# Optimization experiments

Measured on AMD Instinct MI355X. Metric: run time of the kernel, lower is better.

Reference implementation:

```python
import jax, jax.numpy as jnp
import numpy as np

B, N, T = 8, 8192, 2048
CW, DW = 1024, 256  # encoder_width (c_dim), decoder hidden_size
NBLK = 5
EPS = 1e-5


def setup_inputs() -> dict:
    key = jax.random.key(0)
    ks = jax.random.split(key, 32)
    pts = jax.random.normal(ks[0], (B, N, 3), dtype=jnp.float32) * 5.0
    drop = jax.random.bernoulli(ks[1], 0.3, (B, N))
    pts = pts.at[..., 0].set(jnp.where(drop, -100.0, pts[..., 0]))
    rgb = jax.random.uniform(ks[2], (B, N, 3), dtype=jnp.float32)
    query_coords = jax.random.normal(ks[3], (B, T, 3), dtype=jnp.float32) * 5.0
    s = lambda k, shp: jax.random.normal(k, shp, dtype=jnp.float32) * 0.02
    inp = {
        "pts": pts, "rgb": rgb, "query_coords": query_coords,
        # DumbPointnet: pointwise MLP (6->CW->CW) + max pool over points
        "enc_W1": s(ks[4], (6, CW)), "enc_b1": jnp.zeros((CW,), jnp.float32),
        "enc_W2": s(ks[5], (CW, CW)), "enc_b2": jnp.zeros((CW,), jnp.float32),
        # DecoderBatchNorm
        "fc_p_W": s(ks[6], (3, DW)), "fc_p_b": jnp.zeros((DW,), jnp.float32),
        "blk_Wg0": s(ks[7], (NBLK, CW, DW)), "blk_bg0": jnp.ones((NBLK, DW), jnp.float32),
        "blk_Wb0": s(ks[8], (NBLK, CW, DW)), "blk_bb0": jnp.zeros((NBLK, DW), jnp.float32),
        "blk_W0": s(ks[9], (NBLK, DW, DW)), "blk_b0": jnp.zeros((NBLK, DW), jnp.float32),
        "blk_Wg1": s(ks[10], (NBLK, CW, DW)), "blk_bg1": jnp.ones((NBLK, DW), jnp.float32),
        "blk_Wb1": s(ks[11], (NBLK, CW, DW)), "blk_bb1": jnp.zeros((NBLK, DW), jnp.float32),
        "blk_W1": s(ks[12], (NBLK, DW, DW)), "blk_b1": jnp.zeros((NBLK, DW), jnp.float32),
        "bn_Wg": s(ks[13], (CW, DW)), "bn_bg": jnp.ones((DW,), jnp.float32),
        "bn_Wb": s(ks[14], (CW, DW)), "bn_bb": jnp.zeros((DW,), jnp.float32),
        "fc_out_W": s(ks[15], (DW, 1)), "fc_out_b": jnp.zeros((1,), jnp.float32),
    }
    return inp


def _cbn(x, c, Wg, bg, Wb, bb):
    # Conditional BatchNorm1d (training-mode batch stats, affine=False core BN).
    # x: (B,T,F), c: (B,CW)
    mean = x.mean(axis=(0, 1))
    var = x.var(axis=(0, 1))
    xn = (x - mean) * jax.lax.rsqrt(var + EPS)
    gamma = c @ Wg + bg  # (B,F)
    beta = c @ Wb + bb
    return gamma[:, None, :] * xn + beta[:, None, :]


def _forward(pts, rgb, query_coords,
             enc_W1, enc_b1, enc_W2, enc_b2,
             fc_p_W, fc_p_b,
             blk_Wg0, blk_bg0, blk_Wb0, blk_bb0, blk_W0, blk_b0,
             blk_Wg1, blk_bg1, blk_Wb1, blk_bb1, blk_W1, blk_b1,
             bn_Wg, bn_bg, bn_Wb, bn_bb, fc_out_W, fc_out_b):
    mask = pts[..., 0] > -50.0  # (B,N) ragged validity mask
    # 99th-percentile of per-point norms over valid points (torch kthvalue semantics,
    # detached via .item() in the original -> stop_gradient).
    nrm = jnp.where(mask, jnp.linalg.norm(pts, axis=-1), jnp.inf)  # (B,N)
    nrm_sorted = jnp.sort(nrm, axis=-1)
    n_valid = mask.sum(axis=-1)  # (B,)
    k = 1 + jnp.round(0.99 * (n_valid - 1).astype(jnp.float32)).astype(jnp.int32)
    p99 = jnp.take_along_axis(nrm_sorted, (k - 1)[:, None], axis=-1)  # (B,1)
    p99 = jax.lax.stop_gradient(p99)
    pts_n = pts / p99[..., None]
    qc = query_coords / p99[..., None]
    # Encoder: pointwise MLP on [pts_n, rgb], masked max-pool over points
    x = jnp.concatenate([pts_n, rgb], axis=-1)  # (B,N,6)
    h = jax.nn.relu(x @ enc_W1 + enc_b1)
    h = jax.nn.relu(h @ enc_W2 + enc_b2)
    h = jnp.where(mask[..., None], h, -jnp.inf)
    c = h.max(axis=1)  # (B,CW)
    # Decoder: fc_p + 5 conditional-BN resnet blocks + final CBN head
    net = qc @ fc_p_W + fc_p_b  # (B,T,DW)
    for i in range(NBLK):
        dx = jax.nn.relu(_cbn(net, c, blk_Wg0[i], blk_bg0[i], blk_Wb0[i], blk_bb0[i])) @ blk_W0[i] + blk_b0[i]
        dx = jax.nn.relu(_cbn(dx, c, blk_Wg1[i], blk_bg1[i], blk_Wb1[i], blk_bb1[i])) @ blk_W1[i] + blk_b1[i]
        net = net + dx
    out = jax.nn.relu(_cbn(net, c, bn_Wg, bn_bg, bn_Wb, bn_bb)) @ fc_out_W + fc_out_b
    return out[..., 0]  # (B,T) logits


def reference(pts, rgb, query_coords,
              enc_W1, enc_b1, enc_W2, enc_b2,
              fc_p_W, fc_p_b,
              blk_Wg0, blk_bg0, blk_Wb0, blk_bb0, blk_W0, blk_b0,
              blk_Wg1, blk_bg1, blk_Wb1, blk_bb1, blk_W1, blk_b1,
              bn_Wg, bn_bg, bn_Wb, bn_bb, fc_out_W, fc_out_b):
    return _forward(pts, rgb, query_coords,
                    enc_W1, enc_b1, enc_W2, enc_b2,
                    fc_p_W, fc_p_b,
                    blk_Wg0, blk_bg0, blk_Wb0, blk_bb0, blk_W0, blk_b0,
                    blk_Wg1, blk_bg1, blk_Wb1, blk_bb1, blk_W1, blk_b1,
                    bn_Wg, bn_bg, bn_Wb, bn_bb, fc_out_W, fc_out_b)
```

## Files before the change

### kernel.cpp

```cpp
#include <hip/hip_runtime.h>
#include <hip/hip_bf16.h>

#define NB   8
#define NPTS 8192
#define NT   2048
#define CWID 1024
#define DWID 256
#define NPBLK 256

using f32x4  = __attribute__((ext_vector_type(4))) float;
using bf16x8 = __attribute__((ext_vector_type(8))) __bf16;
using bf16x4 = __attribute__((ext_vector_type(4))) __bf16;

#define OFF_INV    0u
#define OFF_C      66560u
#define OFF_GB     99328u
#define OFF_STATS  279552u
#define OFF_W2T    1048576u
#define OFF_WT     3145728u
#define OFF_GBP    4456448u
#define OFF_PART   7340032u
#define OFF_IDX    8388608u
#define OFF_NV     8650752u
#define OFF_NET    19922944u
#define OFF_DX     36700160u
#define OFF_H1     19922944u
#define OFF_H1F    67108864u
#define WS_NEEDED  53477376u
#define WS_BIG     201326592u

__device__ __forceinline__ void async_copy16(const void* g, void* l) {
  __builtin_amdgcn_global_load_lds(
      (const __attribute__((address_space(1))) unsigned int*)g,
      (__attribute__((address_space(3))) unsigned int*)l, 16, 0, 0);
}

__global__ __launch_bounds__(1024) void k_p99(
    const float* __restrict__ pts, float* __restrict__ inv_p99,
    int* __restrict__ idx, int* __restrict__ nv, float* __restrict__ c)
{
  const int b = blockIdx.x;
  const int t = threadIdx.x;
  __shared__ unsigned int keys[NPTS];
  __shared__ int whist[16][256];
  __shared__ int hist[256];
  __shared__ int s_cnt, s_kleft;
  __shared__ unsigned int s_prefix;

  c[b*CWID + t] = 0.f;
  if (t == 0) s_cnt = 0;
  __syncthreads();

  for (int n = t; n < NPTS; n += 1024) {
    const float x = pts[(b*NPTS + n)*3 + 0];
    const float y = pts[(b*NPTS + n)*3 + 1];
    const float z = pts[(b*NPTS + n)*3 + 2];
    const bool v = x > -50.f;
    unsigned int key = 0x7F800000u;
    if (v) {
      key = __float_as_uint(sqrtf(x*x + y*y + z*z));
      const int slot = atomicAdd(&s_cnt, 1);
      idx[b*NPTS + slot] = n;
    }
    keys[n] = key;
  }
  __syncthreads();
  if (t == 0) {
    nv[b] = s_cnt;
    s_kleft = 1 + (int)rintf(0.99f * (float)(s_cnt - 1));
    s_prefix = 0u;
  }
  __syncthreads();

  const int w = t >> 6;
  for (int pass = 0; pass < 4; ++pass) {
    const int shift = 24 - 8*pass;
    const unsigned int pref = s_prefix;
    for (int i = t; i < 16*256; i += 1024) ((int*)whist)[i] = 0;
    __syncthreads();
    for (int n = t; n < NPTS; n += 1024) {
      const unsigned int key = keys[n];
      const bool m = (pass == 0) || ((key >> (shift + 8)) == (pref >> (shift + 8)));
      if (m) atomicAdd(&whist[w][(key >> shift) & 255], 1);
    }
    __syncthreads();
    if (t < 256) { int h = 0; for (int ww = 0; ww < 16; ++ww) h += whist[ww][t]; hist[t] = h; }
    __syncthreads();
    if (t < 64) {
      const int kl = s_kleft;
      const int s0 = hist[t*4+0], s1 = hist[t*4+1], s2 = hist[t*4+2], s3 = hist[t*4+3];
      const int sl = s0 + s1 + s2 + s3;
      int p = sl;
      #pragma unroll
      for (int o = 1; o < 64; o <<= 1) { const int v = __shfl_up(p, o); if (t >= o) p += v; }
      const unsigned long long bl = __ballot(p >= kl);
      const int L = (int)(__ffsll((unsigned long long)bl) - 1);
      if (t == L) {
        int c0 = p - sl;
        int bin = t*4;
        if (c0 + s0 < kl) { c0 += s0; ++bin;
          if (c0 + s1 < kl) { c0 += s1; ++bin;
            if (c0 + s2 < kl) { c0 += s2; ++bin; } } }
        s_prefix = pref | ((unsigned int)bin << shift);
        s_kleft = kl - c0;
      }
    }
    __syncthreads();
  }
  if (t == 0) inv_p99[b] = 1.0f / __uint_as_float(s_prefix);
}

__global__ __launch_bounds__(256) void k_prep(
    const float* __restrict__ w2, __hip_bfloat16* __restrict__ w2t,
    const float* __restrict__ W0, const float* __restrict__ W1,
    __hip_bfloat16* __restrict__ wt)
{
  __shared__ float tile[64][65];
  const int bid = blockIdx.x;
  const int t = threadIdx.x;
  const int cc = t & 63, rq = t >> 6;
  if (bid < 256) {
    const int kb = (bid >> 4) * 64, nb = (bid & 15) * 64;
    #pragma unroll
    for (int i = 0; i < 16; ++i) {
      const int r = i*4 + rq;
      tile[r][cc] = w2[(kb + r)*CWID + nb + cc];
    }
    __syncthreads();
    #pragma unroll
    for (int i = 0; i < 16; ++i) {
      const int r = i*4 + rq;
      w2t[(size_t)(nb + r)*CWID + kb + cc] = __float2bfloat16(tile[cc][r]);
    }
  } else {
    const int idx = bid - 256;
    const int s = idx >> 4;
    const int kb = ((idx >> 2) & 3) * 64, nb = (idx & 3) * 64;
    const float* src = (s < 5) ? (W0 + (size_t)s*DWID*DWID) : (W1 + (size_t)(s-5)*DWID*DWID);
    #pragma unroll
    for (int i = 0; i < 16; ++i) {
      const int r = i*4 + rq;
      tile[r][cc] = src[(kb + r)*DWID + nb + cc];
    }
    __syncthreads();
    #pragma unroll
    for (int i = 0; i < 16; ++i) {
      const int r = i*4 + rq;
      wt[(size_t)s*DWID*DWID + (size_t)(nb + r)*DWID + kb + cc] = __float2bfloat16(tile[cc][r]);
    }
  }
}

#define E1R 16
__global__ __launch_bounds__(256) void k_enc1(
    const float* __restrict__ pts, const float* __restrict__ rgb,
    const float* __restrict__ inv_p99, const int* __restrict__ idx,
    const int* __restrict__ nv,
    const float* __restrict__ W1, const float* __restrict__ b1,
    __hip_bfloat16* __restrict__ h1, int b0)
{
  __shared__ float xs[E1R][6];
  const int z = blockIdx.y;
  const int b = b0 + z;
  const int nvb = nv[b];
  const int r0 = blockIdx.x * E1R;
  if (r0 >= ((nvb + 127) & ~127)) return;
  const int t = threadIdx.x;
  __hip_bfloat16* dst = h1 + (size_t)z*NPTS*CWID;
  if (t < E1R*6) {
    const int m = t / 6, j = t % 6;
    const int row = r0 + m;
    float val = 0.f;
    if (row < nvb) {
      const int gi = b*NPTS + idx[b*NPTS + row];
      const float inv = inv_p99[b];
      val = (j < 3) ? pts[gi*3 + j] * inv : rgb[gi*3 + j - 3];
    }
    xs[m][j] = val;
  }
  __syncthreads();
  #pragma unroll
  for (int k = 0; k < E1R/2; ++k) {
    const int ci = k*256 + t;
    const int m = ci >> 7;
    const bool vrow = (r0 + m) < nvb;
    const int coff = (ci & 127) * 8;
    const float x0 = xs[m][0], x1 = xs[m][1], x2 = xs[m][2];
    const float x3 = xs[m][3], x4 = xs[m][4], x5 = xs[m][5];
    f32x4 aA = *reinterpret_cast<const f32x4*>(&b1[coff]);
    f32x4 aB = *reinterpret_cast<const f32x4*>(&b1[coff + 4]);
    aA = aA + *reinterpret_cast<const f32x4*>(&W1[0*CWID + coff]) * x0;
    aB = aB + *reinterpret_cast<const f32x4*>(&W1[0*CWID + coff + 4]) * x0;
    aA = aA + *reinterpret_cast<const f32x4*>(&W1[1*CWID + coff]) * x1;
    aB = aB + *reinterpret_cast<const f32x4*>(&W1[1*CWID + coff + 4]) * x1;
    aA = aA + *reinterpret_cast<const f32x4*>(&W1[2*CWID + coff]) * x2;
    aB = aB + *reinterpret_cast<const f32x4*>(&W1[2*CWID + coff + 4]) * x2;
    aA = aA + *reinterpret_cast<const f32x4*>(&W1[3*CWID + coff]) * x3;
    aB = aB + *reinterpret_cast<const f32x4*>(&W1[3*CWID + coff + 4]) * x3;
    aA = aA + *reinterpret_cast<const f32x4*>(&W1[4*CWID + coff]) * x4;
    aB = aB + *reinterpret_cast<const f32x4*>(&W1[4*CWID + coff + 4]) * x4;
    aA = aA + *reinterpret_cast<const f32x4*>(&W1[5*CWID + coff]) * x5;
    aB = aB + *reinterpret_cast<const f32x4*>(&W1[5*CWID + coff + 4]) * x5;
    bf16x8 pk;
    #pragma unroll
    for (int u = 0; u < 4; ++u) pk[u]   = vrow ? (__bf16)fmaxf(aA[u], 0.f) : (__bf16)0.f;
    #pragma unroll
    for (int u = 0; u < 4; ++u) pk[4+u] = vrow ? (__bf16)fmaxf(aB[u], 0.f) : (__bf16)0.f;
    *reinterpret_cast<bf16x8*>(&dst[(size_t)(r0 + m)*CWID + coff]) = pk;
  }
}

#define EBM 128
#define EBN 256
#define EBK 64

__global__ __launch_bounds__(512) void k_enc2(
    const __hip_bfloat16* __restrict__ h1,
    const __hip_bfloat16* __restrict__ w2t,
    const float* __restrict__ b2,
    const int* __restrict__ nv,
    float* __restrict__ c, int b0)
{
  __shared__ __align__(16) __hip_bfloat16 As[EBM*EBK];
  __shared__ __align__(16) __hip_bfloat16 Bs[EBN*EBK];
  const int t = threadIdx.x;
  const int lane = t & 63, wid = t >> 6;
  const int wm = wid >> 2, wn = wid & 3;
  const int m0 = blockIdx.x * EBM;
  const int n0 = blockIdx.y * EBN;
  const int z  = blockIdx.z;
  const int b  = b0 + z;
  const int nvb = nv[b];
  if (m0 >= ((nvb + 127) & ~127)) return;
  const __hip_bfloat16* h1b = h1 + (size_t)z*NPTS*CWID;

  f32x4 acc[4][4] = {};

  for (int kt = 0; kt < 16; ++kt) {
    {
      const int k0_ = kt*EBK;
      #pragma unroll
      for (int qq = 0; qq < 2; ++qq) {
        const int cib = qq*512 + wid*64;
        const int ci  = cib + lane;
        const int rw  = ci >> 3;
        const int oct = (ci & 7) ^ (rw & 7);
        async_copy16(h1b + (size_t)(m0 + rw)*CWID + k0_ + oct*8,
                     (__hip_bfloat16*)As + cib*8);
      }
      #pragma unroll
      for (int qq = 0; qq < 4; ++qq) {
        const int cib = qq*512 + wid*64;
        const int ci  = cib + lane;
        const int rw  = ci >> 3;
        const int oct = (ci & 7) ^ (rw & 7);
        async_copy16(w2t + (size_t)(n0 + rw)*CWID + k0_ + oct*8,
                     (__hip_bfloat16*)Bs + cib*8);
      }
    }
    __syncthreads();
    #pragma unroll
    for (int ks = 0; ks < 2; ++ks) {
      const int ke = ks*32 + (lane >> 4)*8;
      const int ao = ke >> 3;
      bf16x8 a[4], bfr[4];
      #pragma unroll
      for (int f = 0; f < 4; ++f) {
        const int ar = wm*64 + f*16 + (lane & 15);
        const int br = wn*64 + f*16 + (lane & 15);
        a[f]   = *reinterpret_cast<const bf16x8*>((char*)As + (ar*8 + (ao ^ (ar & 7)))*16);
        bfr[f] = *reinterpret_cast<const bf16x8*>((char*)Bs + (br*8 + (ao ^ (br & 7)))*16);
      }
      #pragma unroll
      for (int fm = 0; fm < 4; ++fm)
        #pragma unroll
        for (int fn = 0; fn < 4; ++fn)
          acc[fm][fn] = __builtin_amdgcn_mfma_f32_16x16x32_bf16(a[fm], bfr[fn], acc[fm][fn], 0, 0, 0);
    }
    __syncthreads();
  }

  const int rbase = (lane >> 4)*4;
  #pragma unroll
  for (int fn = 0; fn < 4; ++fn) {
    const int gn = n0 + wn*64 + fn*16 + (lane & 15);
    const float bv = b2[gn];
    float mx = 0.f;
    #pragma unroll
    for (int fm = 0; fm < 4; ++fm) {
      const int gmb = m0 + wm*64 + fm*16 + rbase;
      #pragma unroll
      for (int r = 0; r < 4; ++r) {
        const float v = fmaxf(acc[fm][fn][r] + bv, 0.f);
        if (gmb + r < nvb) mx = fmaxf(mx, v);
      }
    }
    mx = fmaxf(mx, __shfl_xor(mx, 16));
    mx = fmaxf(mx, __shfl_xor(mx, 32));
    if ((lane >> 4) == 0)
      atomicMax((int*)(c + b*CWID + gn), __float_as_int(mx));
  }
}

__global__ __launch_bounds__(256) void k_gbp(
    const float* __restrict__ c,
    const float* __restrict__ Wg0, const float* __restrict__ Wb0,
    const float* __restrict__ Wg1, const float* __restrict__ Wb1,
    const float* __restrict__ bnWg, const float* __restrict__ bnWb,
    float* __restrict__ gbp)
{
  __shared__ float cs[8][64];
  __shared__ float red[4][8][256];
  const int s  = blockIdx.y;
  const int kc = blockIdx.x;
  const int k0 = kc * 64;
  const int t  = threadIdx.x;

  const float* W;
  if      (s < 5)  W = Wg0 + (size_t)s*CWID*DWID;
  else if (s < 10) W = Wb0 + (size_t)(s-5)*CWID*DWID;
  else if (s < 15) W = Wg1 + (size_t)(s-10)*CWID*DWID;
  else if (s < 20) W = Wb1 + (size_t)(s-15)*CWID*DWID;
  else if (s == 20) W = bnWg;
  else              W = bnWb;

  {
    const int i0 = t*2;
    cs[i0 >> 6][i0 & 63]         = c[(i0 >> 6)*CWID + k0 + (i0 & 63)];
    cs[(i0+1) >> 6][(i0+1) & 63] = c[((i0+1) >> 6)*CWID + k0 + ((i0+1) & 63)];
  }
  __syncthreads();

  const int sub = t >> 6;
  const int c0  = (t & 63) * 4;
  f32x4 acc[8] = {};
  #pragma unroll
  for (int i = 0; i < 16; ++i) {
    const int kk = sub*16 + i;
    const f32x4 w = *reinterpret_cast<const f32x4*>(&W[(size_t)(k0 + kk)*DWID + c0]);
    #pragma unroll
    for (int b = 0; b < 8; ++b) acc[b] = acc[b] + w * cs[b][kk];
  }
  #pragma unroll
  for (int b = 0; b < 8; ++b)
    *reinterpret_cast<f32x4*>(&red[sub][b][c0]) = acc[b];
  __syncthreads();
  for (int b = 0; b < 8; ++b) {
    const float v = red[0][b][t] + red[1][b][t] + red[2][b][t] + red[3][b][t];
    gbp[(((size_t)s*16 + kc)*8 + b)*DWID + t] = v;
  }
}

__global__ __launch_bounds__(256) void k_gbf(
    const float* __restrict__ gbp,
    const float* __restrict__ bg0, const float* __restrict__ bb0,
    const float* __restrict__ bg1, const float* __restrict__ bb1,
    const float* __restrict__ bnbg, const float* __restrict__ bnbb,
    float* __restrict__ gb)
{
  const int s = blockIdx.x;
  const int t = threadIdx.x;
  const float* bias;
  if      (s < 5)  bias = bg0 + s*DWID;
  else if (s < 10) bias = bb0 + (s-5)*DWID;
  else if (s < 15) bias = bg1 + (s-10)*DWID;
  else if (s < 20) bias = bb1 + (s-15)*DWID;
  else if (s == 20) bias = bnbg;
  else              bias = bnbb;
  const float bv = bias[t];
  for (int b = 0; b < 8; ++b) {
    float acc = bv;
    #pragma unroll
    for (int kc = 0; kc < 16; ++kc)
      acc += gbp[(((size_t)s*16 + kc)*8 + b)*DWID + t];
    gb[((size_t)s*8 + b)*DWID + t] = acc;
  }
}

__global__ __launch_bounds__(256) void k_fcp2(
    const float* __restrict__ qc, const float* __restrict__ inv_p99,
    const float* __restrict__ W, const float* __restrict__ bias,
    __hip_bfloat16* __restrict__ net, float* __restrict__ part)
{
  __shared__ float qs[192];
  const int blk = blockIdx.x;
  const int r0 = blk * 64;
  const int b = r0 >> 11;
  const int t = threadIdx.x;
  if (t < 192) qs[t] = qc[(size_t)r0*3 + t] * inv_p99[b];
  __syncthreads();
  const float w0 = W[t], w1 = W[DWID + t], w2 = W[2*DWID + t];
  const float bv = bias[t];
  float s = 0.f, q = 0.f;
  for (int m = 0; m < 64; ++m) {
    const float v = bv + qs[m*3]*w0 + qs[m*3+1]*w1 + qs[m*3+2]*w2;
    net[(size_t)(r0 + m)*DWID + t] = __float2bfloat16(v);
    s += v; q += v*v;
  }
  part[(size_t)t*NPBLK + blk] = s;
  part[(size_t)(256 + t)*NPBLK + blk] = q;
}

__global__ __launch_bounds__(256) void k_statf(
    const float* __restrict__ part, float* __restrict__ stats)
{
  const int t = threadIdx.x;
  const int j = t >> 5;
  const int lane = t & 31;
  const int col = blockIdx.x * 8 + j;
  const float* ps = part + (size_t)col*NPBLK;
  const float* pq = part + (size_t)(256 + col)*NPBLK;
  f32x4 sv = {}, qv = {};
  #pragma unroll
  for (int i = 0; i < 2; ++i) {
    sv = sv + *reinterpret_cast<const f32x4*>(ps + i*128 + lane*4);
    qv = qv + *reinterpret_cast<const f32x4*>(pq + i*128 + lane*4);
  }
  float s = (sv[0]+sv[1]) + (sv[2]+sv[3]);
  float q = (qv[0]+qv[1]) + (qv[2]+qv[3]);
  #pragma unroll
  for (int o = 16; o > 0; o >>= 1) { s += __shfl_down(s, o); q += __shfl_down(q, o); }
  if (lane == 0) {
    const float mean = s * (1.f/16384.f);
    const float var  = q * (1.f/16384.f) - mean*mean;
    stats[col] = mean;
    stats[256 + col] = rsqrtf(var + 1e-5f);
  }
}

__global__ __launch_bounds__(256) void k_cbnmm(
    const __hip_bfloat16* __restrict__ X, const float* __restrict__ stats,
    const float* __restrict__ gb, int gslot, int bslot,
    const __hip_bfloat16* __restrict__ wt,
    const float* __restrict__ bias,
    __hip_bfloat16* __restrict__ out, int addmode, float* __restrict__ part)
{
  __shared__ __align__(16) __hip_bfloat16 xs[64 * 256];
  __shared__ float sred[4][2][128];
  const int t = threadIdx.x;
  const int blk = blockIdx.x;
  const int r0 = blk * 64;
  const int bb = r0 >> 11;

  {
    const int cq = (t & 63) * 4;
    const f32x4 mn = *reinterpret_cast<const f32x4*>(&stats[cq]);
    const f32x4 rs = *reinterpret_cast<const f32x4*>(&stats[256 + cq]);
    const f32x4 g  = *reinterpret_cast<const f32x4*>(&gb[((size_t)gslot*8 + bb)*DWID + cq]);
    const f32x4 be = *reinterpret_cast<const f32x4*>(&gb[((size_t)bslot*8 + bb)*DWID + cq]);
    const int rbase = t >> 6;
    #pragma unroll
    for (int j = 0; j < 16; ++j) {
      const int r = rbase + j*4;
      const bf16x4 xv = *reinterpret_cast<const bf16x4*>(&X[(size_t)(r0 + r)*DWID + cq]);
      bf16x4 h;
      #pragma unroll
      for (int jj = 0; jj < 4; ++jj)
        h[jj] = (__bf16)fmaxf(0.f, ((float)xv[jj] - mn[jj])*rs[jj]*g[jj] + be[jj]);
      const int grp = (cq >> 3) ^ (r & 7);
      *reinterpret_cast<bf16x4*>((char*)xs + r*512 + grp*16 + (cq & 7)*2) = h;
    }
  }
  __syncthreads();

  const int lane = t & 63, wid = t >> 6;
  const int wm = wid >> 1, wn = wid & 1;
  f32x4 acc[2][8] = {};
  #pragma unroll
  for (int kstep = 0; kstep < 8; ++kstep) {
    const int ke = kstep*32 + (lane >> 4)*8;
    bf16x8 a[2], bfr[8];
    #pragma unroll
    for (int fm = 0; fm < 2; ++fm) {
      const int row = wm*32 + fm*16 + (lane & 15);
      a[fm] = *reinterpret_cast<const bf16x8*>(
          (char*)xs + row*512 + (((ke >> 3) ^ (row & 7))*16));
    }
    #pragma unroll
    for (int fn = 0; fn < 8; ++fn) {
      const int n = wn*128 + fn*16 + (lane & 15);
      bfr[fn] = *reinterpret_cast<const bf16x8*>(&wt[(size_t)n*DWID + ke]);
    }
    #pragma unroll
    for (int fm = 0; fm < 2; ++fm)
      #pragma unroll
      for (int fn = 0; fn < 8; ++fn)
        acc[fm][fn] = __builtin_amdgcn_mfma_f32_16x16x32_bf16(a[fm], bfr[fn], acc[fm][fn], 0, 0, 0);
  }

  const int rb = (lane >> 4) * 4;
  #pragma unroll
  for (int fn = 0; fn < 8; ++fn) {
    const int gn = wn*128 + fn*16 + (lane & 15);
    const float bv = bias[gn];
    float s = 0.f, q = 0.f;
    #pragma unroll
    for (int fm = 0; fm < 2; ++fm) {
      const size_t row0 = (size_t)r0 + wm*32 + fm*16 + rb;
      #pragma unroll
      for (int r = 0; r < 4; ++r) {
        float v = acc[fm][fn][r] + bv;
        if (addmode) v += (float)out[(row0 + r)*DWID + gn];
        out[(row0 + r)*DWID + gn] = __float2bfloat16(v);
        s += v; q += v*v;
      }
    }
    s += __shfl_xor(s, 16); s += __shfl_xor(s, 32);
    q += __shfl_xor(q, 16); q += __shfl_xor(q, 32);
    if ((lane >> 4) == 0) {
      sred[wid][0][fn*16 + (lane & 15)] = s;
      sred[wid][1][fn*16 + (lane & 15)] = q;
    }
  }
  __syncthreads();
  {
    const int col = t;
    const int wn2 = col >> 7, cl = col & 127;
    const float s = sred[wn2][0][cl] + sred[2 + wn2][0][cl];
    const float q = sred[wn2][1][cl] + sred[2 + wn2][1][cl];
    part[(size_t)col*NPBLK + blk] = s;
    part[(size_t)(256 + col)*NPBLK + blk] = q;
  }
}

__global__ __launch_bounds__(256) void k_final(
    const __hip_bfloat16* __restrict__ net, const float* __restrict__ stats,
    const float* __restrict__ gb, const float* __restrict__ fcW,
    const float* __restrict__ fcb, float* __restrict__ out)
{
  const int wid = threadIdx.x >> 6, lane = threadIdx.x & 63;
  const int m = blockIdx.x*4 + wid;
  const int b = m >> 11;
  const int f0 = lane*4;
  const bf16x4 xv = *reinterpret_cast<const bf16x4*>(&net[(size_t)m*DWID + f0]);
  const f32x4 mn = *reinterpret_cast<const f32x4*>(&stats[f0]);
  const f32x4 rs = *reinterpret_cast<const f32x4*>(&stats[256 + f0]);
  const f32x4 g  = *reinterpret_cast<const f32x4*>(&gb[(20*8 + (size_t)b)*DWID + f0]);
  const f32x4 be = *reinterpret_cast<const f32x4*>(&gb[(21*8 + (size_t)b)*DWID + f0]);
  const f32x4 w  = *reinterpret_cast<const f32x4*>(&fcW[f0]);
  float s = 0.f;
  #pragma unroll
  for (int j = 0; j < 4; ++j)
    s += fmaxf(0.f, ((float)xv[j] - mn[j])*rs[j]*g[j] + be[j]) * w[j];
  #pragma unroll
  for (int o = 32; o > 0; o >>= 1) s += __shfl_down(s, o);
  if (lane == 0) out[m] = s + fcb[0];
}

extern "C" void kernel_launch(void* const* d_in, const int* in_sizes, int n_in,
                              void* d_out, int out_size, void* d_ws, size_t ws_size,
                              hipStream_t stream) {
  (void)in_sizes; (void)n_in; (void)out_size;
  if (ws_size < WS_NEEDED) return;

  const float* pts    = (const float*)d_in[0];
  const float* rgb    = (const float*)d_in[1];
  const float* qc     = (const float*)d_in[2];
  const float* enc_W1 = (const float*)d_in[3];
  const float* enc_b1 = (const float*)d_in[4];
  const float* enc_W2 = (const float*)d_in[5];
  const float* enc_b2 = (const float*)d_in[6];
  const float* fc_p_W = (const float*)d_in[7];
  const float* fc_p_b = (const float*)d_in[8];
  const float* Wg0 = (const float*)d_in[9];
  const float* bg0 = (const float*)d_in[10];
  const float* Wb0 = (const float*)d_in[11];
  const float* bb0 = (const float*)d_in[12];
  const float* W0  = (const float*)d_in[13];
  const float* b0  = (const float*)d_in[14];
  const float* Wg1 = (const float*)d_in[15];
  const float* bg1 = (const float*)d_in[16];
  const float* Wb1 = (const float*)d_in[17];
  const float* bb1 = (const float*)d_in[18];
  const float* W1  = (const float*)d_in[19];
  const float* b1  = (const float*)d_in[20];
  const float* bnWg = (const float*)d_in[21];
  const float* bnbg = (const float*)d_in[22];
  const float* bnWb = (const float*)d_in[23];
  const float* bnbb = (const float*)d_in[24];
  const float* fcoW = (const float*)d_in[25];
  const float* fcob = (const float*)d_in[26];
  float* out = (float*)d_out;

  char* ws = (char*)d_ws;
  float* inv_p99 = (float*)(ws + OFF_INV);
  float* c      = (float*)(ws + OFF_C);
  float* gbuf   = (float*)(ws + OFF_GB);
  float* stats  = (float*)(ws + OFF_STATS);
  __hip_bfloat16* w2t = (__hip_bfloat16*)(ws + OFF_W2T);
  __hip_bfloat16* wt  = (__hip_bfloat16*)(ws + OFF_WT);
  float* gbp  = (float*)(ws + OFF_GBP);
  float* part = (float*)(ws + OFF_PART);
  int*   idx  = (int*)(ws + OFF_IDX);
  int*   nvp  = (int*)(ws + OFF_NV);
  __hip_bfloat16* net = (__hip_bfloat16*)(ws + OFF_NET);
  __hip_bfloat16* dx  = (__hip_bfloat16*)(ws + OFF_DX);

  k_p99<<<NB, 1024, 0, stream>>>(pts, inv_p99, idx, nvp, c);
  k_prep<<<416, 256, 0, stream>>>(enc_W2, w2t, W0, W1, wt);

  if (ws_size >= WS_BIG) {
    __hip_bfloat16* h1f = (__hip_bfloat16*)(ws + OFF_H1F);
    k_enc1<<<dim3(NPTS/E1R, NB), 256, 0, stream>>>(pts, rgb, inv_p99, idx, nvp,
                                                   enc_W1, enc_b1, h1f, 0);
    k_enc2<<<dim3(NPTS/EBM, CWID/EBN, NB), 512, 0, stream>>>(h1f, w2t, enc_b2,
                                                             nvp, c, 0);
  } else {
    __hip_bfloat16* h1 = (__hip_bfloat16*)(ws + OFF_H1);
    for (int bp = 0; bp < 4; ++bp) {
      k_enc1<<<dim3(NPTS/E1R, 2), 256, 0, stream>>>(pts, rgb, inv_p99, idx, nvp,
                                                    enc_W1, enc_b1, h1, bp*2);
      k_enc2<<<dim3(NPTS/EBM, CWID/EBN, 2), 512, 0, stream>>>(h1, w2t, enc_b2,
                                                              nvp, c, bp*2);
    }
  }

  k_gbp<<<dim3(16,22), 256, 0, stream>>>(c, Wg0, Wb0, Wg1, Wb1, bnWg, bnWb, gbp);
  k_gbf<<<22, 256, 0, stream>>>(gbp, bg0, bb0, bg1, bb1, bnbg, bnbb, gbuf);

  k_fcp2<<<NPBLK, 256, 0, stream>>>(qc, inv_p99, fc_p_W, fc_p_b, net, part);
  k_statf<<<32, 256, 0, stream>>>(part, stats);
  for (int i = 0; i < 5; ++i) {
    k_cbnmm<<<NPBLK, 256, 0, stream>>>(net, stats, gbuf, i, 5+i,
                                       wt + (size_t)i*DWID*DWID, b0 + i*DWID, dx, 0, part);
    k_statf<<<32, 256, 0, stream>>>(part, stats);
    k_cbnmm<<<NPBLK, 256, 0, stream>>>(dx, stats, gbuf, 10+i, 15+i,
                                       wt + (size_t)(5+i)*DWID*DWID, b1 + i*DWID, net, 1, part);
    k_statf<<<32, 256, 0, stream>>>(part, stats);
  }
  k_final<<<NB*NT/4, 256, 0, stream>>>(net, stats, gbuf, fcoW, fcob, out);
}
```

Before: 406.6 us.

## Fuse first encoder layer into second-layer GEMM, computing h1 tiles in LDS

The pointwise 6->1024 first encoder layer now runs inside the encoder GEMM kernel. Each block computes its 128x64 activation tile per K-step from six per-row inputs and writes it straight into the swizzled LDS A buffer, so the large bf16 h1 intermediate is never written to or read back from global memory. This also removes the separate k_enc1 launches and the workspace-size branch. The cost is that h1 is recomputed once for each of the 4 N-tile blocks, and W1/b1 loads are added to the GEMM main loop.

```diff
diff --git a/kernel.cpp b/kernel.cpp
--- a/kernel.cpp
+++ b/kernel.cpp
@@ -24,10 +24,7 @@
 #define OFF_NV     8650752u
 #define OFF_NET    19922944u
 #define OFF_DX     36700160u
-#define OFF_H1     19922944u
-#define OFF_H1F    67108864u
 #define WS_NEEDED  53477376u
-#define WS_BIG     201326592u
 
 __device__ __forceinline__ void async_copy16(const void* g, void* l) {
   __builtin_amdgcn_global_load_lds(
@@ -151,103 +148,58 @@
   }
 }
 
-#define E1R 16
-__global__ __launch_bounds__(256) void k_enc1(
+#define EBM 128
+#define EBN 256
+#define EBK 64
+
+__global__ __launch_bounds__(512) void k_enc2f(
     const float* __restrict__ pts, const float* __restrict__ rgb,
     const float* __restrict__ inv_p99, const int* __restrict__ idx,
     const int* __restrict__ nv,
     const float* __restrict__ W1, const float* __restrict__ b1,
-    __hip_bfloat16* __restrict__ h1, int b0)
-{
-  __shared__ float xs[E1R][6];
-  const int z = blockIdx.y;
-  const int b = b0 + z;
-  const int nvb = nv[b];
-  const int r0 = blockIdx.x * E1R;
-  if (r0 >= ((nvb + 127) & ~127)) return;
-  const int t = threadIdx.x;
-  __hip_bfloat16* dst = h1 + (size_t)z*NPTS*CWID;
-  if (t < E1R*6) {
-    const int m = t / 6, j = t % 6;
-    const int row = r0 + m;
-    float val = 0.f;
-    if (row < nvb) {
-      const int gi = b*NPTS + idx[b*NPTS + row];
-      const float inv = inv_p99[b];
-      val = (j < 3) ? pts[gi*3 + j] * inv : rgb[gi*3 + j - 3];
-    }
-    xs[m][j] = val;
-  }
-  __syncthreads();
-  #pragma unroll
-  for (int k = 0; k < E1R/2; ++k) {
-    const int ci = k*256 + t;
-    const int m = ci >> 7;
-    const bool vrow = (r0 + m) < nvb;
-    const int coff = (ci & 127) * 8;
-    const float x0 = xs[m][0], x1 = xs[m][1], x2 = xs[m][2];
-    const float x3 = xs[m][3], x4 = xs[m][4], x5 = xs[m][5];
-    f32x4 aA = *reinterpret_cast<const f32x4*>(&b1[coff]);
-    f32x4 aB = *reinterpret_cast<const f32x4*>(&b1[coff + 4]);
-    aA = aA + *reinterpret_cast<const f32x4*>(&W1[0*CWID + coff]) * x0;
-    aB = aB + *reinterpret_cast<const f32x4*>(&W1[0*CWID + coff + 4]) * x0;
-    aA = aA + *reinterpret_cast<const f32x4*>(&W1[1*CWID + coff]) * x1;
-    aB = aB + *reinterpret_cast<const f32x4*>(&W1[1*CWID + coff + 4]) * x1;
-    aA = aA + *reinterpret_cast<const f32x4*>(&W1[2*CWID + coff]) * x2;
-    aB = aB + *reinterpret_cast<const f32x4*>(&W1[2*CWID + coff + 4]) * x2;
-    aA = aA + *reinterpret_cast<const f32x4*>(&W1[3*CWID + coff]) * x3;
-    aB = aB + *reinterpret_cast<const f32x4*>(&W1[3*CWID + coff + 4]) * x3;
-    aA = aA + *reinterpret_cast<const f32x4*>(&W1[4*CWID + coff]) * x4;
-    aB = aB + *reinterpret_cast<const f32x4*>(&W1[4*CWID + coff + 4]) * x4;
-    aA = aA + *reinterpret_cast<const f32x4*>(&W1[5*CWID + coff]) * x5;
-    aB = aB + *reinterpret_cast<const f32x4*>(&W1[5*CWID + coff + 4]) * x5;
-    bf16x8 pk;
-    #pragma unroll
-    for (int u = 0; u < 4; ++u) pk[u]   = vrow ? (__bf16)fmaxf(aA[u], 0.f) : (__bf16)0.f;
-    #pragma unroll
-    for (int u = 0; u < 4; ++u) pk[4+u] = vrow ? (__bf16)fmaxf(aB[u], 0.f) : (__bf16)0.f;
-    *reinterpret_cast<bf16x8*>(&dst[(size_t)(r0 + m)*CWID + coff]) = pk;
-  }
-}
-
-#define EBM 128
-#define EBN 256
-#define EBK 64
-
-__global__ __launch_bounds__(512) void k_enc2(
-    const __hip_bfloat16* __restrict__ h1,
     const __hip_bfloat16* __restrict__ w2t,
     const float* __restrict__ b2,
-    const int* __restrict__ nv,
-    float* __restrict__ c, int b0)
+    float* __restrict__ c)
 {
   __shared__ __align__(16) __hip_bfloat16 As[EBM*EBK];
   __shared__ __align__(16) __hip_bfloat16 Bs[EBN*EBK];
+  __shared__ float xs[EBM][6];
   const int t = threadIdx.x;
   const int lane = t & 63, wid = t >> 6;
   const int wm = wid >> 2, wn = wid & 3;
   const int m0 = blockIdx.x * EBM;
   const int n0 = blockIdx.y * EBN;
-  const int z  = blockIdx.z;
-  const int b  = b0 + z;
+  const int b  = blockIdx.z;
   const int nvb = nv[b];
   if (m0 >= ((nvb + 127) & ~127)) return;
-  const __hip_bfloat16* h1b = h1 + (size_t)z*NPTS*CWID;
+
+  {
+    const float inv = inv_p99[b];
+    for (int i = t; i < EBM*6; i += 512) {
+      const int r = i / 6, j = i % 6;
+      float val = 0.f;
+      if (m0 + r < nvb) {
+        const int gi = b*NPTS + idx[b*NPTS + m0 + r];
+        val = (j < 3) ? pts[gi*3 + j]*inv : rgb[gi*3 + (j-3)];
+      }
+      xs[r][j] = val;
+    }
+  }
+  __syncthreads();
+
+  const int arow = t & 127;
+  const int o0   = (t >> 7) * 2;
+  float xr[6];
+  #pragma unroll
+  for (int j = 0; j < 6; ++j) xr[j] = xs[arow][j];
+  const int wA0 = (arow*8 + ( o0      ^ (arow & 7))) * 16;
+  const int wA1 = (arow*8 + ((o0 + 1) ^ (arow & 7))) * 16;
 
   f32x4 acc[4][4] = {};
 
   for (int kt = 0; kt < 16; ++kt) {
     {
       const int k0_ = kt*EBK;
-      #pragma unroll
-      for (int qq = 0; qq < 2; ++qq) {
-        const int cib = qq*512 + wid*64;
-        const int ci  = cib + lane;
-        const int rw  = ci >> 3;
-        const int oct = (ci & 7) ^ (rw & 7);
-        async_copy16(h1b + (size_t)(m0 + rw)*CWID + k0_ + oct*8,
-                     (__hip_bfloat16*)As + cib*8);
-      }
       #pragma unroll
       for (int qq = 0; qq < 4; ++qq) {
         const int cib = qq*512 + wid*64;
@@ -257,6 +209,31 @@
         async_copy16(w2t + (size_t)(n0 + rw)*CWID + k0_ + oct*8,
                      (__hip_bfloat16*)Bs + cib*8);
       }
+    }
+    {
+      const int kb = kt*EBK + o0*8;
+      f32x4 c0A = *reinterpret_cast<const f32x4*>(&b1[kb]);
+      f32x4 c0B = *reinterpret_cast<const f32x4*>(&b1[kb + 4]);
+      f32x4 c1A = *reinterpret_cast<const f32x4*>(&b1[kb + 8]);
+      f32x4 c1B = *reinterpret_cast<const f32x4*>(&b1[kb + 12]);
+      #pragma unroll
+      for (int j = 0; j < 6; ++j) {
+        const float xv = xr[j];
+        c0A = c0A + *reinterpret_cast<const f32x4*>(&W1[j*CWID + kb])      * xv;
+        c0B = c0B + *reinterpret_cast<const f32x4*>(&W1[j*CWID + kb + 4])  * xv;
+        c1A = c1A + *reinterpret_cast<const f32x4*>(&W1[j*CWID + kb + 8])  * xv;
+        c1B = c1B + *reinterpret_cast<const f32x4*>(&W1[j*CWID + kb + 12]) * xv;
+      }
+      bf16x8 p0, p1;
+      #pragma unroll
+      for (int u = 0; u < 4; ++u) {
+        p0[u]   = (__bf16)fmaxf(c0A[u], 0.f);
+        p0[4+u] = (__bf16)fmaxf(c0B[u], 0.f);
+        p1[u]   = (__bf16)fmaxf(c1A[u], 0.f);
+        p1[4+u] = (__bf16)fmaxf(c1B[u], 0.f);
+      }
+      *reinterpret_cast<bf16x8*>((char*)As + wA0) = p0;
+      *reinterpret_cast<bf16x8*>((char*)As + wA1) = p1;
     }
     __syncthreads();
     #pragma unroll
@@ -599,21 +576,8 @@
   k_p99<<<NB, 1024, 0, stream>>>(pts, inv_p99, idx, nvp, c);
   k_prep<<<416, 256, 0, stream>>>(enc_W2, w2t, W0, W1, wt);
 
-  if (ws_size >= WS_BIG) {
-    __hip_bfloat16* h1f = (__hip_bfloat16*)(ws + OFF_H1F);
-    k_enc1<<<dim3(NPTS/E1R, NB), 256, 0, stream>>>(pts, rgb, inv_p99, idx, nvp,
-                                                   enc_W1, enc_b1, h1f, 0);
-    k_enc2<<<dim3(NPTS/EBM, CWID/EBN, NB), 512, 0, stream>>>(h1f, w2t, enc_b2,
-                                                             nvp, c, 0);
-  } else {
-    __hip_bfloat16* h1 = (__hip_bfloat16*)(ws + OFF_H1);
-    for (int bp = 0; bp < 4; ++bp) {
-      k_enc1<<<dim3(NPTS/E1R, 2), 256, 0, stream>>>(pts, rgb, inv_p99, idx, nvp,
-                                                    enc_W1, enc_b1, h1, bp*2);
-      k_enc2<<<dim3(NPTS/EBM, CWID/EBN, 2), 512, 0, stream>>>(h1, w2t, enc_b2,
-                                                              nvp, c, bp*2);
-    }
-  }
+  k_enc2f<<<dim3(NPTS/EBM, CWID/EBN, NB), 512, 0, stream>>>(
+      pts, rgb, inv_p99, idx, nvp, enc_W1, enc_b1, w2t, enc_b2, c);
 
   k_gbp<<<dim3(16,22), 256, 0, stream>>>(c, Wg0, Wb0, Wg1, Wb1, bnWg, bnWb, gbp);
   k_gbf<<<22, 256, 0, stream>>>(gbp, bg0, bb0, bg1, bb1, bnbg, bnbb, gbuf);
```

Result: slower. 639.4 us (+57.3%).

## Double-buffer encoder GEMM LDS tiles with async prefetch two stages ahead

Applied to the files above, without the earlier changes.

Halves the K tile of the encoder second-layer GEMM and adds two LDS buffers, so global-to-LDS async copies for tile kt+2 are issued while MFMAs run on tile kt. Explicit vmcnt waits and raw barriers replace __syncthreads. The LDS swizzle is reworked for the 32-wide K tile, packing two rows per 128-byte line. The goal is to hide global load latency, at the cost of twice as many loop iterations and barriers, and reliance on a hand-counted vmcnt.

```diff
diff --git a/kernel.cpp b/kernel.cpp
--- a/kernel.cpp
+++ b/kernel.cpp
@@ -212,7 +212,7 @@
 
 #define EBM 128
 #define EBN 256
-#define EBK 64
+#define EBK 32
 
 __global__ __launch_bounds__(512) void k_enc2(
     const __hip_bfloat16* __restrict__ h1,
@@ -221,8 +221,8 @@
     const int* __restrict__ nv,
     float* __restrict__ c, int b0)
 {
-  __shared__ __align__(16) __hip_bfloat16 As[EBM*EBK];
-  __shared__ __align__(16) __hip_bfloat16 Bs[EBN*EBK];
+  __shared__ __align__(16) __hip_bfloat16 As[2][EBM*EBK];
+  __shared__ __align__(16) __hip_bfloat16 Bs[2][EBN*EBK];
   const int t = threadIdx.x;
   const int lane = t & 63, wid = t >> 6;
   const int wm = wid >> 2, wn = wid & 3;
@@ -234,42 +234,51 @@
   if (m0 >= ((nvb + 127) & ~127)) return;
   const __hip_bfloat16* h1b = h1 + (size_t)z*NPTS*CWID;
 
+  #define STAGE(buf, kt) do {                                              \
+    const int k0_ = (kt)*EBK;                                              \
+    {                    \
+      const int u  = t;                                                    \
+      const int rp = u >> 3, x_ = u & 7;                                   \
+      const int sub = x_ ^ (rp & 7);                                       \
+      const int r   = (rp << 1) | (sub >> 2);                              \
+      const int oct = sub & 3;                                             \
+      async_copy16(h1b + (size_t)(m0 + r)*CWID + k0_ + oct*8,              \
+                   (__hip_bfloat16*)As[buf] + (size_t)u*8);                \
+    }                                                                      \
+    _Pragma("unroll")                                                      \
+    for (int qq = 0; qq < 2; ++qq) {      \
+      const int u  = qq*512 + t;                                           \
+      const int rp = u >> 3, x_ = u & 7;                                   \
+      const int sub = x_ ^ (rp & 7);                                       \
+      const int r   = (rp << 1) | (sub >> 2);                              \
+      const int oct = sub & 3;                                             \
+      async_copy16(w2t + (size_t)(n0 + r)*CWID + k0_ + oct*8,              \
+                   (__hip_bfloat16*)Bs[buf] + (size_t)u*8);                \
+    }                                                                      \
+  } while (0)
+
   f32x4 acc[4][4] = {};
 
-  for (int kt = 0; kt < 16; ++kt) {
+  STAGE(0, 0);
+  STAGE(1, 1);
+  const int ke = (lane >> 4) * 8;
+  const int ao = ke >> 3;
+  for (int kt = 0; kt < 32; ++kt) {
+    const int cur = kt & 1;
+    if (kt < 31) { asm volatile("s_waitcnt vmcnt(3)" ::: "memory"); }
+    else         { asm volatile("s_waitcnt vmcnt(0)" ::: "memory"); }
+    __builtin_amdgcn_s_barrier();
+    __builtin_amdgcn_sched_barrier(0);
     {
-      const int k0_ = kt*EBK;
-      #pragma unroll
-      for (int qq = 0; qq < 2; ++qq) {
-        const int cib = qq*512 + wid*64;
-        const int ci  = cib + lane;
-        const int rw  = ci >> 3;
-        const int oct = (ci & 7) ^ (rw & 7);
-        async_copy16(h1b + (size_t)(m0 + rw)*CWID + k0_ + oct*8,
-                     (__hip_bfloat16*)As + cib*8);
-      }
-      #pragma unroll
-      for (int qq = 0; qq < 4; ++qq) {
-        const int cib = qq*512 + wid*64;
-        const int ci  = cib + lane;
-        const int rw  = ci >> 3;
-        const int oct = (ci & 7) ^ (rw & 7);
-        async_copy16(w2t + (size_t)(n0 + rw)*CWID + k0_ + oct*8,
-                     (__hip_bfloat16*)Bs + cib*8);
-      }
-    }
-    __syncthreads();
-    #pragma unroll
-    for (int ks = 0; ks < 2; ++ks) {
-      const int ke = ks*32 + (lane >> 4)*8;
-      const int ao = ke >> 3;
       bf16x8 a[4], bfr[4];
       #pragma unroll
       for (int f = 0; f < 4; ++f) {
         const int ar = wm*64 + f*16 + (lane & 15);
         const int br = wn*64 + f*16 + (lane & 15);
-        a[f]   = *reinterpret_cast<const bf16x8*>((char*)As + (ar*8 + (ao ^ (ar & 7)))*16);
-        bfr[f] = *reinterpret_cast<const bf16x8*>((char*)Bs + (br*8 + (ao ^ (br & 7)))*16);
+        const int ua = (ar >> 1)*8 + (((((ar & 1) << 2) | ao)) ^ ((ar >> 1) & 7));
+        const int ub = (br >> 1)*8 + (((((br & 1) << 2) | ao)) ^ ((br >> 1) & 7));
+        a[f]   = *reinterpret_cast<const bf16x8*>((char*)As[cur] + ua*16);
+        bfr[f] = *reinterpret_cast<const bf16x8*>((char*)Bs[cur] + ub*16);
       }
       #pragma unroll
       for (int fm = 0; fm < 4; ++fm)
@@ -277,8 +286,12 @@
         for (int fn = 0; fn < 4; ++fn)
           acc[fm][fn] = __builtin_amdgcn_mfma_f32_16x16x32_bf16(a[fm], bfr[fn], acc[fm][fn], 0, 0, 0);
     }
-    __syncthreads();
-  }
+    __builtin_amdgcn_sched_barrier(0);
+    __builtin_amdgcn_s_barrier();
+    __builtin_amdgcn_sched_barrier(0);
+    if (kt < 30) STAGE(cur, kt + 2);
+  }
+  #undef STAGE
 
   const int rbase = (lane >> 4)*4;
   #pragma unroll
```

New measurement: 428.9 us. 5.5% more time.
